# Optimization experiments

Hardware: AMD Instinct MI355X
Metric: run time of the kernel (lower is better)

Reference implementation:

```python
import jax, jax.numpy as jnp
import numpy as np

VIS_DIM = 4096
HIDDEN_D = 4096
EMB_DIM = 512
B = 128
N_NEG = 2048


def setup_inputs() -> dict:
    key = jax.random.key(0)
    k = jax.random.split(key, 7)
    vfs = jax.random.normal(k[0], (B, VIS_DIM), dtype=jnp.float32)
    p_lfs = jax.random.normal(k[1], (B, EMB_DIM), dtype=jnp.float32)
    n_lfs = jax.random.normal(k[2], (N_NEG, EMB_DIM), dtype=jnp.float32)
    # Linear params (PyTorch layout: W [out, in], y = x @ W.T + b)
    s_h = 1.0 / np.sqrt(VIS_DIM)
    s_e = 1.0 / np.sqrt(HIDDEN_D)
    W_h = jax.random.uniform(k[3], (HIDDEN_D, VIS_DIM), jnp.float32, -s_h, s_h)
    b_h = jax.random.uniform(k[4], (HIDDEN_D,), jnp.float32, -s_h, s_h)
    W_e = jax.random.uniform(k[5], (EMB_DIM, HIDDEN_D), jnp.float32, -s_e, s_e)
    b_e = jax.random.uniform(k[6], (EMB_DIM,), jnp.float32, -s_e, s_e)
    return {"vfs": vfs, "p_lfs": p_lfs, "n_lfs": n_lfs,
            "W_h": W_h, "b_h": b_h, "W_e": W_e, "b_e": b_e}


def _partial_order_sim(hypers, hypos):
    # -||relu(hypers - hypos)||_2 reduced over the last axis
    act = jax.nn.relu(hypers - hypos)
    return -jnp.sqrt(jnp.sum(act * act, axis=-1))


def reference(vfs, p_lfs, n_lfs, W_h, b_h, W_e, b_e):
    # Two plain Linears (NO ReLU in between, matching the original forward)
    vf_hidden = vfs @ W_h.T + b_h            # [B, 4096]
    vf_emb = vf_hidden @ W_e.T + b_e          # [B, emb]
    # positive score per sample
    p_scores = _partial_order_sim(p_lfs, vf_emb)                    # [B]
    # negative scores, batched over all samples at once (replaces per-sample loop)
    n_scores = _partial_order_sim(n_lfs[None, :, :], vf_emb[:, None, :])  # [B, N]
    score_stack = jnp.concatenate([p_scores[:, None], n_scores], axis=1)  # [B, N+1]
    return score_stack
```

## Files before the change

### kernel.cpp

```cpp
#include <hip/hip_runtime.h>
#include <hip/hip_bf16.h>

#define B_N  128
#define VIS  4096
#define HID  4096
#define EMB  512
#define NNEG 2048
#define OUTN (NNEG + 1)
#define SPLIT1 8
#define SPLIT2 16

using f32x4  = __attribute__((ext_vector_type(4))) float;
using f32x2  = __attribute__((ext_vector_type(2))) float;
using bf16x8 = __attribute__((ext_vector_type(8))) short;

static __device__ __forceinline__ unsigned pk2bf(float x, float y) {
  union { __hip_bfloat162 h; unsigned u; } c;
  c.h = __float22bfloat162_rn(make_float2(x, y));
  return c.u;
}

#define PIPE_BARRIER() __asm__ volatile("s_waitcnt lgkmcnt(0)\n\ts_barrier" ::: "memory")

__global__ __launch_bounds__(256) void prep_kernel(
    const float* __restrict__ src, unsigned short* __restrict__ dst,
    float* __restrict__ emb) {
  const int idx = blockIdx.x * 256 + threadIdx.x;
  float4 a = ((const float4*)src)[idx * 2];
  float4 b = ((const float4*)src)[idx * 2 + 1];
  uint4 pk;
  pk.x = pk2bf(a.x, a.y); pk.y = pk2bf(a.z, a.w);
  pk.z = pk2bf(b.x, b.y); pk.w = pk2bf(b.z, b.w);
  ((uint4*)dst)[idx] = pk;
  if (idx < (B_N * EMB / 4))
    ((float4*)emb)[idx] = make_float4(0.f, 0.f, 0.f, 0.f);
}

__global__ __launch_bounds__(512, 4) void gemm1_kernel(
    const unsigned short* __restrict__ Abf, const float* __restrict__ Wh,
    const float* __restrict__ bh, float* __restrict__ Hp) {
  const int n0    = blockIdx.x * 64;
  const int kbase = blockIdx.y * 512;

  __shared__ __align__(16) unsigned short Ws[2][64 * 64];

  const int t = threadIdx.x, w = t >> 6, lane = t & 63;
  const int m_lane = lane & 15, kq = lane >> 4;
  f32x4 acc[4] = {};

  const int wr = t >> 3, wg = t & 7;
  const float* Wg = Wh + (size_t)(n0 + wr) * VIS + kbase + wg * 8;
  const int wofs = wr * 64 + ((wg ^ (wr & 7)) * 8);

  const unsigned short* Ag = Abf + (size_t)(w * 16 + m_lane) * VIS + kbase + kq * 8;

  float4 wva[8], wvb[8];
#pragma unroll
  for (int i = 0; i < 8; ++i) {
    wva[i] = *(const float4*)(Wg + i * 64);
    wvb[i] = *(const float4*)(Wg + i * 64 + 4);
  }

  bf16x8 av[3][2];
  av[0][0] = *(const bf16x8*)(Ag);
  av[0][1] = *(const bf16x8*)(Ag + 32);
  av[1][0] = *(const bf16x8*)(Ag + 64);
  av[1][1] = *(const bf16x8*)(Ag + 96);

  {
    uint4 pk;
    pk.x = pk2bf(wva[0].x, wva[0].y); pk.y = pk2bf(wva[0].z, wva[0].w);
    pk.z = pk2bf(wvb[0].x, wvb[0].y); pk.w = pk2bf(wvb[0].z, wvb[0].w);
    *(uint4*)&Ws[0][wofs] = pk;
  }
  PIPE_BARRIER();

#pragma unroll
  for (int k = 0; k < 8; ++k) {
    const int cur = k & 1;
    if (k + 2 < 8) {
      av[(k + 2) % 3][0] = *(const bf16x8*)(Ag + (k + 2) * 64);
      av[(k + 2) % 3][1] = *(const bf16x8*)(Ag + (k + 2) * 64 + 32);
    }
    if (k + 1 < 8) {
      uint4 pk;
      pk.x = pk2bf(wva[k + 1].x, wva[k + 1].y); pk.y = pk2bf(wva[k + 1].z, wva[k + 1].w);
      pk.z = pk2bf(wvb[k + 1].x, wvb[k + 1].y); pk.w = pk2bf(wvb[k + 1].z, wvb[k + 1].w);
      *(uint4*)&Ws[1 - cur][wofs] = pk;
    }
#pragma unroll
    for (int ks = 0; ks < 2; ++ks) {
      const int Gk = ks * 4 + kq;
      const bf16x8 a = av[k % 3][ks];
#pragma unroll
      for (int ni = 0; ni < 4; ++ni) {
        const int c = m_lane + ni * 16;
        bf16x8 b = *(const bf16x8*)&Ws[cur][c * 64 + ((Gk ^ (c & 7)) * 8)];
        acc[ni] = __builtin_amdgcn_mfma_f32_16x16x32_bf16(a, b, acc[ni], 0, 0, 0);
      }
    }
    PIPE_BARRIER();
  }

  float* Pd = Hp + (size_t)blockIdx.y * (B_N * HID);
  const int rq = (lane >> 4) * 4;
#pragma unroll
  for (int ni = 0; ni < 4; ++ni) {
    const int ng = n0 + ni * 16 + m_lane;
    const float bias = (blockIdx.y == 0) ? bh[ng] : 0.0f;
#pragma unroll
    for (int r = 0; r < 4; ++r)
      Pd[(size_t)(w * 16 + rq + r) * HID + ng] = acc[ni][r] + bias;
  }
}

__global__ __launch_bounds__(256) void cvt_kernel(
    const float* __restrict__ Hp, unsigned short* __restrict__ dst) {
  const int idx = blockIdx.x * 256 + threadIdx.x;
  const size_t PS = (size_t)B_N * HID;
  float4 a = ((const float4*)Hp)[idx * 2];
  float4 b = ((const float4*)Hp)[idx * 2 + 1];
#pragma unroll
  for (int p = 1; p < SPLIT1; ++p) {
    float4 ap = ((const float4*)(Hp + p * PS))[idx * 2];
    float4 bp = ((const float4*)(Hp + p * PS))[idx * 2 + 1];
    a.x += ap.x; a.y += ap.y; a.z += ap.z; a.w += ap.w;
    b.x += bp.x; b.y += bp.y; b.z += bp.z; b.w += bp.w;
  }
  uint4 pk;
  pk.x = pk2bf(a.x, a.y); pk.y = pk2bf(a.z, a.w);
  pk.z = pk2bf(b.x, b.y); pk.w = pk2bf(b.z, b.w);
  ((uint4*)dst)[idx] = pk;
}

__global__ __launch_bounds__(512, 4) void gemm2_kernel(
    const unsigned short* __restrict__ Hbf, const float* __restrict__ We,
    const float* __restrict__ be, float* __restrict__ emb) {
  const int n0    = blockIdx.x * 16;
  const int kbase = blockIdx.y * 256;

  __shared__ __align__(16) unsigned short Ws[2][16 * 64];

  const int t = threadIdx.x, w = t >> 6, lane = t & 63;
  const int m_lane = lane & 15, kq = lane >> 4;
  f32x4 acc = {};

  const int wr = t >> 5, e = (t & 31) * 2;
  const float* Wg = We + (size_t)(n0 + wr) * HID + kbase + e;
  const int wofs = wr * 64 + (((e >> 3) ^ (wr & 7)) * 8) + (e & 7);

  const unsigned short* Ag = Hbf + (size_t)(w * 16 + m_lane) * HID + kbase + kq * 8;

  float2 wv[4];
#pragma unroll
  for (int i = 0; i < 4; ++i) wv[i] = *(const float2*)(Wg + i * 64);

  bf16x8 av[3][2];
  av[0][0] = *(const bf16x8*)(Ag);
  av[0][1] = *(const bf16x8*)(Ag + 32);
  av[1][0] = *(const bf16x8*)(Ag + 64);
  av[1][1] = *(const bf16x8*)(Ag + 96);

  *(unsigned*)&Ws[0][wofs] = pk2bf(wv[0].x, wv[0].y);
  PIPE_BARRIER();

#pragma unroll
  for (int k = 0; k < 4; ++k) {
    const int cur = k & 1;
    if (k + 2 < 4) {
      av[(k + 2) % 3][0] = *(const bf16x8*)(Ag + (k + 2) * 64);
      av[(k + 2) % 3][1] = *(const bf16x8*)(Ag + (k + 2) * 64 + 32);
    }
    if (k + 1 < 4) {
      const float2 wc = wv[k + 1];
      *(unsigned*)&Ws[1 - cur][wofs] = pk2bf(wc.x, wc.y);
    }
#pragma unroll
    for (int ks = 0; ks < 2; ++ks) {
      const int Gk = ks * 4 + kq;
      bf16x8 b0 = *(const bf16x8*)&Ws[cur][m_lane * 64 + ((Gk ^ (m_lane & 7)) * 8)];
      acc = __builtin_amdgcn_mfma_f32_16x16x32_bf16(av[k % 3][ks], b0, acc, 0, 0, 0);
    }
    PIPE_BARRIER();
  }

  const int rq = (lane >> 4) * 4;
  const int ng = n0 + m_lane;
  const float bias = (blockIdx.y == 0) ? be[ng] : 0.0f;
#pragma unroll
  for (int r = 0; r < 4; ++r)
    atomicAdd(&emb[(w * 16 + rq + r) * EMB + ng], acc[r] + bias);
}

__global__ __launch_bounds__(256, 2) void score_kernel(
    const float* __restrict__ emb, const float* __restrict__ n_lfs,
    const float* __restrict__ p_lfs, float* __restrict__ out) {
  const int bx = blockIdx.x;
  const int t = threadIdx.x;
  const int s = t & 15, tb = t >> 4;
  const f32x2 z2 = {0.f, 0.f};

  if (bx < 1024) {
    const int nc = bx >> 3, bt = bx & 7;
    const int n0 = nc * 16, b0 = bt * 16;
    __shared__ __align__(16) float nl[16 * 576];
#pragma unroll
    for (int i = 0; i < 8; ++i) {
      const int f = t + i * 256;
      const int r = f >> 7, o4 = f & 127;
      float4 v = *(const float4*)(n_lfs + (size_t)(n0 + r) * EMB + o4 * 4);
      *(float4*)&nl[r * 576 + (o4 >> 3) * 36 + (o4 & 7) * 4] = v;
    }
    const float* eb = emb + (size_t)(b0 + tb) * EMB + s * 32;
    f32x2 ev[16];
#pragma unroll
    for (int i = 0; i < 8; ++i) {
      float4 v = *(const float4*)(eb + i * 4);
      ev[2 * i]     = (f32x2){v.x, v.y};
      ev[2 * i + 1] = (f32x2){v.z, v.w};
    }
    __syncthreads();

    for (int j = 0; j < 16; ++j) {
      const float* nr = &nl[j * 576 + s * 36];
      f32x2 a0 = z2, a1 = z2;
#pragma unroll
      for (int i = 0; i < 8; ++i) {
        float4 nv = *(const float4*)(nr + i * 4);
        f32x2 d0 = (f32x2){nv.x, nv.y} - ev[2 * i];
        f32x2 d1 = (f32x2){nv.z, nv.w} - ev[2 * i + 1];
        d0 = __builtin_elementwise_max(d0, z2);
        d1 = __builtin_elementwise_max(d1, z2);
        a0 = __builtin_elementwise_fma(d0, d0, a0);
        a1 = __builtin_elementwise_fma(d1, d1, a1);
      }
      float ss = (a0.x + a0.y) + (a1.x + a1.y);
      ss += __shfl_xor(ss, 1);
      ss += __shfl_xor(ss, 2);
      ss += __shfl_xor(ss, 4);
      ss += __shfl_xor(ss, 8);
      if (s == 0) out[(size_t)(b0 + tb) * OUTN + 1 + n0 + j] = -sqrtf(ss);
    }
  } else {
    const int b = (bx - 1024) * 16 + tb;
    const float* eb = emb + (size_t)b * EMB + s * 32;
    const float* pb = p_lfs + (size_t)b * EMB + s * 32;
    f32x2 a0 = z2, a1 = z2;
#pragma unroll
    for (int i = 0; i < 8; ++i) {
      float4 pv = *(const float4*)(pb + i * 4);
      float4 ev = *(const float4*)(eb + i * 4);
      f32x2 d0 = (f32x2){pv.x, pv.y} - (f32x2){ev.x, ev.y};
      f32x2 d1 = (f32x2){pv.z, pv.w} - (f32x2){ev.z, ev.w};
      d0 = __builtin_elementwise_max(d0, z2);
      d1 = __builtin_elementwise_max(d1, z2);
      a0 = __builtin_elementwise_fma(d0, d0, a0);
      a1 = __builtin_elementwise_fma(d1, d1, a1);
    }
    float ss = (a0.x + a0.y) + (a1.x + a1.y);
    ss += __shfl_xor(ss, 1);
    ss += __shfl_xor(ss, 2);
    ss += __shfl_xor(ss, 4);
    ss += __shfl_xor(ss, 8);
    if (s == 0) out[(size_t)b * OUTN] = -sqrtf(ss);
  }
}

extern "C" void kernel_launch(void* const* d_in, const int* in_sizes, int n_in,
                              void* d_out, int out_size, void* d_ws, size_t ws_size,
                              hipStream_t stream) {
  const float* vfs   = (const float*)d_in[0];
  const float* p_lfs = (const float*)d_in[1];
  const float* n_lfs = (const float*)d_in[2];
  const float* W_h   = (const float*)d_in[3];
  const float* b_h   = (const float*)d_in[4];
  const float* W_e   = (const float*)d_in[5];
  const float* b_e   = (const float*)d_in[6];
  float* out = (float*)d_out;

  char* ws = (char*)d_ws;
  float*          Hp  = (float*)ws;
  float*          emb = (float*)(ws + (16u << 20));
  unsigned short* Abf = (unsigned short*)(ws + (16u << 20) + (256u << 10));
  unsigned short* Hbf = (unsigned short*)(ws + (17u << 20) + (256u << 10));

  prep_kernel<<<256, 256, 0, stream>>>(vfs, Abf, emb);
  gemm1_kernel<<<dim3(HID / 64, SPLIT1), 512, 0, stream>>>(Abf, W_h, b_h, Hp);
  cvt_kernel<<<256, 256, 0, stream>>>(Hp, Hbf);
  gemm2_kernel<<<dim3(EMB / 16, SPLIT2), 512, 0, stream>>>(Hbf, W_e, b_e, emb);
  score_kernel<<<1032, 256, 0, stream>>>(emb, n_lfs, p_lfs, out);
}
```

Measured before the change: 155.0 us.

## Fuse all five stages into one persistent kernel with grid barriers

Replaces the prep, two GEMM, reduce-convert and score kernels with a single persistent kernel of 512 blocks that separates the stages with atomic-counter grid barriers. A memset resets the barrier counters before each launch. This removes four kernel launch gaps and their tail effects, at the cost of global spin barriers and a deadlock risk if all 512 blocks cannot be resident at once. The score stage is regrouped so each block handles 32 batch rows by 16 negatives, giving 512 blocks.

```diff
diff --git a/kernel.cpp b/kernel.cpp
--- a/kernel.cpp
+++ b/kernel.cpp
@@ -9,6 +9,7 @@
 #define OUTN (NNEG + 1)
 #define SPLIT1 8
 #define SPLIT2 16
+#define NBLK 512u
 
 using f32x4  = __attribute__((ext_vector_type(4))) float;
 using f32x2  = __attribute__((ext_vector_type(2))) float;
@@ -22,191 +23,197 @@
 
 #define PIPE_BARRIER() __asm__ volatile("s_waitcnt lgkmcnt(0)\n\ts_barrier" ::: "memory")
 
-__global__ __launch_bounds__(256) void prep_kernel(
-    const float* __restrict__ src, unsigned short* __restrict__ dst,
-    float* __restrict__ emb) {
-  const int idx = blockIdx.x * 256 + threadIdx.x;
-  float4 a = ((const float4*)src)[idx * 2];
-  float4 b = ((const float4*)src)[idx * 2 + 1];
-  uint4 pk;
-  pk.x = pk2bf(a.x, a.y); pk.y = pk2bf(a.z, a.w);
-  pk.z = pk2bf(b.x, b.y); pk.w = pk2bf(b.z, b.w);
-  ((uint4*)dst)[idx] = pk;
-  if (idx < (B_N * EMB / 4))
-    ((float4*)emb)[idx] = make_float4(0.f, 0.f, 0.f, 0.f);
+static __device__ __forceinline__ void gbar(unsigned* bar, int ph) {
+  __syncthreads();
+  if (threadIdx.x == 0) {
+    __threadfence();
+    __hip_atomic_fetch_add(&bar[ph], 1u, __ATOMIC_RELEASE, __HIP_MEMORY_SCOPE_AGENT);
+    while (__hip_atomic_load(&bar[ph], __ATOMIC_ACQUIRE, __HIP_MEMORY_SCOPE_AGENT) < NBLK)
+      __builtin_amdgcn_s_sleep(2);
+    __threadfence();
+  }
+  __syncthreads();
 }
 
-__global__ __launch_bounds__(512, 4) void gemm1_kernel(
-    const unsigned short* __restrict__ Abf, const float* __restrict__ Wh,
-    const float* __restrict__ bh, float* __restrict__ Hp) {
-  const int n0    = blockIdx.x * 64;
-  const int kbase = blockIdx.y * 512;
-
-  __shared__ __align__(16) unsigned short Ws[2][64 * 64];
-
-  const int t = threadIdx.x, w = t >> 6, lane = t & 63;
-  const int m_lane = lane & 15, kq = lane >> 4;
-  f32x4 acc[4] = {};
-
-  const int wr = t >> 3, wg = t & 7;
-  const float* Wg = Wh + (size_t)(n0 + wr) * VIS + kbase + wg * 8;
-  const int wofs = wr * 64 + ((wg ^ (wr & 7)) * 8);
-
-  const unsigned short* Ag = Abf + (size_t)(w * 16 + m_lane) * VIS + kbase + kq * 8;
-
-  float4 wva[8], wvb[8];
-#pragma unroll
-  for (int i = 0; i < 8; ++i) {
-    wva[i] = *(const float4*)(Wg + i * 64);
-    wvb[i] = *(const float4*)(Wg + i * 64 + 4);
-  }
-
-  bf16x8 av[3][2];
-  av[0][0] = *(const bf16x8*)(Ag);
-  av[0][1] = *(const bf16x8*)(Ag + 32);
-  av[1][0] = *(const bf16x8*)(Ag + 64);
-  av[1][1] = *(const bf16x8*)(Ag + 96);
-
-  {
-    uint4 pk;
-    pk.x = pk2bf(wva[0].x, wva[0].y); pk.y = pk2bf(wva[0].z, wva[0].w);
-    pk.z = pk2bf(wvb[0].x, wvb[0].y); pk.w = pk2bf(wvb[0].z, wvb[0].w);
-    *(uint4*)&Ws[0][wofs] = pk;
-  }
-  PIPE_BARRIER();
-
-#pragma unroll
-  for (int k = 0; k < 8; ++k) {
-    const int cur = k & 1;
-    if (k + 2 < 8) {
-      av[(k + 2) % 3][0] = *(const bf16x8*)(Ag + (k + 2) * 64);
-      av[(k + 2) % 3][1] = *(const bf16x8*)(Ag + (k + 2) * 64 + 32);
-    }
-    if (k + 1 < 8) {
+__global__ __launch_bounds__(512, 4) void mega_kernel(
+    const float* __restrict__ vfs, const float* __restrict__ p_lfs,
+    const float* __restrict__ n_lfs, const float* __restrict__ Wh,
+    const float* __restrict__ bh, const float* __restrict__ We,
+    const float* __restrict__ be, float* __restrict__ out,
+    float* __restrict__ Hp, float* __restrict__ emb,
+    unsigned short* __restrict__ Abf, unsigned short* __restrict__ Hbf,
+    unsigned* __restrict__ bar) {
+
+  __shared__ __align__(16) char smem[16 * 576 * 4];
+
+  const int bid = blockIdx.x, t = threadIdx.x;
+  const int gid = bid * 512 + t;
+
+  {
+    float2 a = ((const float2*)vfs)[gid];
+    ((unsigned*)Abf)[gid] = pk2bf(a.x, a.y);
+    if (gid < (B_N * EMB / 4))
+      ((float4*)emb)[gid] = make_float4(0.f, 0.f, 0.f, 0.f);
+  }
+  gbar(bar, 0);
+
+  {
+    const int bx = bid & 63, by = bid >> 6;
+    const int n0    = bx * 64;
+    const int kbase = by * 512;
+    unsigned short* Wsb = (unsigned short*)smem;
+
+    const int w = t >> 6, lane = t & 63;
+    const int m_lane = lane & 15, kq = lane >> 4;
+    f32x4 acc[4] = {};
+
+    const int wr = t >> 3, wg = t & 7;
+    const float* Wg = Wh + (size_t)(n0 + wr) * VIS + kbase + wg * 8;
+    const int wofs = wr * 64 + ((wg ^ (wr & 7)) * 8);
+
+    const unsigned short* Ag = Abf + (size_t)(w * 16 + m_lane) * VIS + kbase + kq * 8;
+
+    float4 wva[8], wvb[8];
+#pragma unroll
+    for (int i = 0; i < 8; ++i) {
+      wva[i] = *(const float4*)(Wg + i * 64);
+      wvb[i] = *(const float4*)(Wg + i * 64 + 4);
+    }
+
+    bf16x8 av[3][2];
+    av[0][0] = *(const bf16x8*)(Ag);
+    av[0][1] = *(const bf16x8*)(Ag + 32);
+    av[1][0] = *(const bf16x8*)(Ag + 64);
+    av[1][1] = *(const bf16x8*)(Ag + 96);
+
+    {
       uint4 pk;
-      pk.x = pk2bf(wva[k + 1].x, wva[k + 1].y); pk.y = pk2bf(wva[k + 1].z, wva[k + 1].w);
-      pk.z = pk2bf(wvb[k + 1].x, wvb[k + 1].y); pk.w = pk2bf(wvb[k + 1].z, wvb[k + 1].w);
-      *(uint4*)&Ws[1 - cur][wofs] = pk;
-    }
-#pragma unroll
-    for (int ks = 0; ks < 2; ++ks) {
-      const int Gk = ks * 4 + kq;
-      const bf16x8 a = av[k % 3][ks];
-#pragma unroll
-      for (int ni = 0; ni < 4; ++ni) {
-        const int c = m_lane + ni * 16;
-        bf16x8 b = *(const bf16x8*)&Ws[cur][c * 64 + ((Gk ^ (c & 7)) * 8)];
-        acc[ni] = __builtin_amdgcn_mfma_f32_16x16x32_bf16(a, b, acc[ni], 0, 0, 0);
-      }
+      pk.x = pk2bf(wva[0].x, wva[0].y); pk.y = pk2bf(wva[0].z, wva[0].w);
+      pk.z = pk2bf(wvb[0].x, wvb[0].y); pk.w = pk2bf(wvb[0].z, wvb[0].w);
+      *(uint4*)&Wsb[wofs] = pk;
     }
     PIPE_BARRIER();
-  }
-
-  float* Pd = Hp + (size_t)blockIdx.y * (B_N * HID);
-  const int rq = (lane >> 4) * 4;
-#pragma unroll
-  for (int ni = 0; ni < 4; ++ni) {
-    const int ng = n0 + ni * 16 + m_lane;
-    const float bias = (blockIdx.y == 0) ? bh[ng] : 0.0f;
+
+#pragma unroll
+    for (int k = 0; k < 8; ++k) {
+      const int cur = k & 1;
+      if (k + 2 < 8) {
+        av[(k + 2) % 3][0] = *(const bf16x8*)(Ag + (k + 2) * 64);
+        av[(k + 2) % 3][1] = *(const bf16x8*)(Ag + (k + 2) * 64 + 32);
+      }
+      if (k + 1 < 8) {
+        uint4 pk;
+        pk.x = pk2bf(wva[k + 1].x, wva[k + 1].y); pk.y = pk2bf(wva[k + 1].z, wva[k + 1].w);
+        pk.z = pk2bf(wvb[k + 1].x, wvb[k + 1].y); pk.w = pk2bf(wvb[k + 1].z, wvb[k + 1].w);
+        *(uint4*)&Wsb[(1 - cur) * 4096 + wofs] = pk;
+      }
+#pragma unroll
+      for (int ks = 0; ks < 2; ++ks) {
+        const int Gk = ks * 4 + kq;
+        const bf16x8 a = av[k % 3][ks];
+#pragma unroll
+        for (int ni = 0; ni < 4; ++ni) {
+          const int c = m_lane + ni * 16;
+          bf16x8 b = *(const bf16x8*)&Wsb[cur * 4096 + c * 64 + ((Gk ^ (c & 7)) * 8)];
+          acc[ni] = __builtin_amdgcn_mfma_f32_16x16x32_bf16(a, b, acc[ni], 0, 0, 0);
+        }
+      }
+      PIPE_BARRIER();
+    }
+
+    float* Pd = Hp + (size_t)by * (B_N * HID);
+    const int rq = (lane >> 4) * 4;
+#pragma unroll
+    for (int ni = 0; ni < 4; ++ni) {
+      const int ng = n0 + ni * 16 + m_lane;
+      const float bias = (by == 0) ? bh[ng] : 0.0f;
+#pragma unroll
+      for (int r = 0; r < 4; ++r)
+        Pd[(size_t)(w * 16 + rq + r) * HID + ng] = acc[ni][r] + bias;
+    }
+  }
+  gbar(bar, 1);
+
+  {
+    const size_t PS2 = (size_t)B_N * HID / 2;
+    const float2* hp2 = (const float2*)Hp;
+    float2 a = hp2[gid];
+#pragma unroll
+    for (int p = 1; p < SPLIT1; ++p) {
+      float2 v = hp2[gid + p * PS2];
+      a.x += v.x; a.y += v.y;
+    }
+    ((unsigned*)Hbf)[gid] = pk2bf(a.x, a.y);
+  }
+  gbar(bar, 2);
+
+  {
+    const int bx = bid & 31, by = bid >> 5;
+    const int n0    = bx * 16;
+    const int kbase = by * 256;
+    unsigned short* Wsb = (unsigned short*)smem;
+
+    const int w = t >> 6, lane = t & 63;
+    const int m_lane = lane & 15, kq = lane >> 4;
+    f32x4 acc = {};
+
+    const int wr = t >> 5, e = (t & 31) * 2;
+    const float* Wg = We + (size_t)(n0 + wr) * HID + kbase + e;
+    const int wofs = wr * 64 + (((e >> 3) ^ (wr & 7)) * 8) + (e & 7);
+
+    const unsigned short* Ag = Hbf + (size_t)(w * 16 + m_lane) * HID + kbase + kq * 8;
+
+    float2 wv[4];
+#pragma unroll
+    for (int i = 0; i < 4; ++i) wv[i] = *(const float2*)(Wg + i * 64);
+
+    bf16x8 av[3][2];
+    av[0][0] = *(const bf16x8*)(Ag);
+    av[0][1] = *(const bf16x8*)(Ag + 32);
+    av[1][0] = *(const bf16x8*)(Ag + 64);
+    av[1][1] = *(const bf16x8*)(Ag + 96);
+
+    *(unsigned*)&Wsb[wofs] = pk2bf(wv[0].x, wv[0].y);
+    PIPE_BARRIER();
+
+#pragma unroll
+    for (int k = 0; k < 4; ++k) {
+      const int cur = k & 1;
+      if (k + 2 < 4) {
+        av[(k + 2) % 3][0] = *(const bf16x8*)(Ag + (k + 2) * 64);
+        av[(k + 2) % 3][1] = *(const bf16x8*)(Ag + (k + 2) * 64 + 32);
+      }
+      if (k + 1 < 4) {
+        const float2 wc = wv[k + 1];
+        *(unsigned*)&Wsb[(1 - cur) * 1024 + wofs] = pk2bf(wc.x, wc.y);
+      }
+#pragma unroll
+      for (int ks = 0; ks < 2; ++ks) {
+        const int Gk = ks * 4 + kq;
+        bf16x8 b0 = *(const bf16x8*)&Wsb[cur * 1024 + m_lane * 64 + ((Gk ^ (m_lane & 7)) * 8)];
+        acc = __builtin_amdgcn_mfma_f32_16x16x32_bf16(av[k % 3][ks], b0, acc, 0, 0, 0);
+      }
+      PIPE_BARRIER();
+    }
+
+    const int rq = (lane >> 4) * 4;
+    const int ng = n0 + m_lane;
+    const float bias = (by == 0) ? be[ng] : 0.0f;
 #pragma unroll
     for (int r = 0; r < 4; ++r)
-      Pd[(size_t)(w * 16 + rq + r) * HID + ng] = acc[ni][r] + bias;
-  }
-}
-
-__global__ __launch_bounds__(256) void cvt_kernel(
-    const float* __restrict__ Hp, unsigned short* __restrict__ dst) {
-  const int idx = blockIdx.x * 256 + threadIdx.x;
-  const size_t PS = (size_t)B_N * HID;
-  float4 a = ((const float4*)Hp)[idx * 2];
-  float4 b = ((const float4*)Hp)[idx * 2 + 1];
-#pragma unroll
-  for (int p = 1; p < SPLIT1; ++p) {
-    float4 ap = ((const float4*)(Hp + p * PS))[idx * 2];
-    float4 bp = ((const float4*)(Hp + p * PS))[idx * 2 + 1];
-    a.x += ap.x; a.y += ap.y; a.z += ap.z; a.w += ap.w;
-    b.x += bp.x; b.y += bp.y; b.z += bp.z; b.w += bp.w;
-  }
-  uint4 pk;
-  pk.x = pk2bf(a.x, a.y); pk.y = pk2bf(a.z, a.w);
-  pk.z = pk2bf(b.x, b.y); pk.w = pk2bf(b.z, b.w);
-  ((uint4*)dst)[idx] = pk;
-}
-
-__global__ __launch_bounds__(512, 4) void gemm2_kernel(
-    const unsigned short* __restrict__ Hbf, const float* __restrict__ We,
-    const float* __restrict__ be, float* __restrict__ emb) {
-  const int n0    = blockIdx.x * 16;
-  const int kbase = blockIdx.y * 256;
-
-  __shared__ __align__(16) unsigned short Ws[2][16 * 64];
-
-  const int t = threadIdx.x, w = t >> 6, lane = t & 63;
-  const int m_lane = lane & 15, kq = lane >> 4;
-  f32x4 acc = {};
-
-  const int wr = t >> 5, e = (t & 31) * 2;
-  const float* Wg = We + (size_t)(n0 + wr) * HID + kbase + e;
-  const int wofs = wr * 64 + (((e >> 3) ^ (wr & 7)) * 8) + (e & 7);
-
-  const unsigned short* Ag = Hbf + (size_t)(w * 16 + m_lane) * HID + kbase + kq * 8;
-
-  float2 wv[4];
-#pragma unroll
-  for (int i = 0; i < 4; ++i) wv[i] = *(const float2*)(Wg + i * 64);
-
-  bf16x8 av[3][2];
-  av[0][0] = *(const bf16x8*)(Ag);
-  av[0][1] = *(const bf16x8*)(Ag + 32);
-  av[1][0] = *(const bf16x8*)(Ag + 64);
-  av[1][1] = *(const bf16x8*)(Ag + 96);
-
-  *(unsigned*)&Ws[0][wofs] = pk2bf(wv[0].x, wv[0].y);
-  PIPE_BARRIER();
-
-#pragma unroll
-  for (int k = 0; k < 4; ++k) {
-    const int cur = k & 1;
-    if (k + 2 < 4) {
-      av[(k + 2) % 3][0] = *(const bf16x8*)(Ag + (k + 2) * 64);
-      av[(k + 2) % 3][1] = *(const bf16x8*)(Ag + (k + 2) * 64 + 32);
-    }
-    if (k + 1 < 4) {
-      const float2 wc = wv[k + 1];
-      *(unsigned*)&Ws[1 - cur][wofs] = pk2bf(wc.x, wc.y);
-    }
-#pragma unroll
-    for (int ks = 0; ks < 2; ++ks) {
-      const int Gk = ks * 4 + kq;
-      bf16x8 b0 = *(const bf16x8*)&Ws[cur][m_lane * 64 + ((Gk ^ (m_lane & 7)) * 8)];
-      acc = __builtin_amdgcn_mfma_f32_16x16x32_bf16(av[k % 3][ks], b0, acc, 0, 0, 0);
-    }
-    PIPE_BARRIER();
-  }
-
-  const int rq = (lane >> 4) * 4;
-  const int ng = n0 + m_lane;
-  const float bias = (blockIdx.y == 0) ? be[ng] : 0.0f;
-#pragma unroll
-  for (int r = 0; r < 4; ++r)
-    atomicAdd(&emb[(w * 16 + rq + r) * EMB + ng], acc[r] + bias);
-}
-
-__global__ __launch_bounds__(256, 2) void score_kernel(
-    const float* __restrict__ emb, const float* __restrict__ n_lfs,
-    const float* __restrict__ p_lfs, float* __restrict__ out) {
-  const int bx = blockIdx.x;
-  const int t = threadIdx.x;
-  const int s = t & 15, tb = t >> 4;
-  const f32x2 z2 = {0.f, 0.f};
-
-  if (bx < 1024) {
-    const int nc = bx >> 3, bt = bx & 7;
-    const int n0 = nc * 16, b0 = bt * 16;
-    __shared__ __align__(16) float nl[16 * 576];
-#pragma unroll
-    for (int i = 0; i < 8; ++i) {
-      const int f = t + i * 256;
+      atomicAdd(&emb[(w * 16 + rq + r) * EMB + ng], acc[r] + bias);
+  }
+  gbar(bar, 3);
+
+  {
+    float* nl = (float*)smem;
+    const int s = t & 15, tb = t >> 4;
+    const int n0 = (bid >> 2) * 16, b0 = (bid & 3) * 32;
+    const f32x2 z2 = {0.f, 0.f};
+
+#pragma unroll
+    for (int i = 0; i < 4; ++i) {
+      const int f = t + i * 512;
       const int r = f >> 7, o4 = f & 127;
       float4 v = *(const float4*)(n_lfs + (size_t)(n0 + r) * EMB + o4 * 4);
       *(float4*)&nl[r * 576 + (o4 >> 3) * 36 + (o4 & 7) * 4] = v;
@@ -241,28 +248,30 @@
       ss += __shfl_xor(ss, 8);
       if (s == 0) out[(size_t)(b0 + tb) * OUTN + 1 + n0 + j] = -sqrtf(ss);
     }
-  } else {
-    const int b = (bx - 1024) * 16 + tb;
-    const float* eb = emb + (size_t)b * EMB + s * 32;
-    const float* pb = p_lfs + (size_t)b * EMB + s * 32;
-    f32x2 a0 = z2, a1 = z2;
-#pragma unroll
-    for (int i = 0; i < 8; ++i) {
-      float4 pv = *(const float4*)(pb + i * 4);
-      float4 ev = *(const float4*)(eb + i * 4);
-      f32x2 d0 = (f32x2){pv.x, pv.y} - (f32x2){ev.x, ev.y};
-      f32x2 d1 = (f32x2){pv.z, pv.w} - (f32x2){ev.z, ev.w};
-      d0 = __builtin_elementwise_max(d0, z2);
-      d1 = __builtin_elementwise_max(d1, z2);
-      a0 = __builtin_elementwise_fma(d0, d0, a0);
-      a1 = __builtin_elementwise_fma(d1, d1, a1);
-    }
-    float ss = (a0.x + a0.y) + (a1.x + a1.y);
-    ss += __shfl_xor(ss, 1);
-    ss += __shfl_xor(ss, 2);
-    ss += __shfl_xor(ss, 4);
-    ss += __shfl_xor(ss, 8);
-    if (s == 0) out[(size_t)b * OUTN] = -sqrtf(ss);
+
+    if (bid < 8 && tb < 16) {
+      const int b = bid * 16 + tb;
+      const float* pb = p_lfs + (size_t)b * EMB + s * 32;
+      const float* ebp = emb + (size_t)b * EMB + s * 32;
+      f32x2 a0 = z2, a1 = z2;
+#pragma unroll
+      for (int i = 0; i < 8; ++i) {
+        float4 pv = *(const float4*)(pb + i * 4);
+        float4 evv = *(const float4*)(ebp + i * 4);
+        f32x2 d0 = (f32x2){pv.x, pv.y} - (f32x2){evv.x, evv.y};
+        f32x2 d1 = (f32x2){pv.z, pv.w} - (f32x2){evv.z, evv.w};
+        d0 = __builtin_elementwise_max(d0, z2);
+        d1 = __builtin_elementwise_max(d1, z2);
+        a0 = __builtin_elementwise_fma(d0, d0, a0);
+        a1 = __builtin_elementwise_fma(d1, d1, a1);
+      }
+      float ss = (a0.x + a0.y) + (a1.x + a1.y);
+      ss += __shfl_xor(ss, 1);
+      ss += __shfl_xor(ss, 2);
+      ss += __shfl_xor(ss, 4);
+      ss += __shfl_xor(ss, 8);
+      if (s == 0) out[(size_t)b * OUTN] = -sqrtf(ss);
+    }
   }
 }
 
@@ -283,10 +292,9 @@
   float*          emb = (float*)(ws + (16u << 20));
   unsigned short* Abf = (unsigned short*)(ws + (16u << 20) + (256u << 10));
   unsigned short* Hbf = (unsigned short*)(ws + (17u << 20) + (256u << 10));
-
-  prep_kernel<<<256, 256, 0, stream>>>(vfs, Abf, emb);
-  gemm1_kernel<<<dim3(HID / 64, SPLIT1), 512, 0, stream>>>(Abf, W_h, b_h, Hp);
-  cvt_kernel<<<256, 256, 0, stream>>>(Hp, Hbf);
-  gemm2_kernel<<<dim3(EMB / 16, SPLIT2), 512, 0, stream>>>(Hbf, W_e, b_e, emb);
-  score_kernel<<<1032, 256, 0, stream>>>(emb, n_lfs, p_lfs, out);
+  unsigned*       bar = (unsigned*)(ws + (18u << 20) + (256u << 10));
+
+  hipMemsetAsync(bar, 0, 4 * sizeof(unsigned), stream);
+  mega_kernel<<<NBLK, 512, 0, stream>>>(vfs, p_lfs, n_lfs, W_h, b_h, W_e, b_e,
+                                        out, Hp, emb, Abf, Hbf, bar);
 }
```

Measured after the change: 451.4 us. +191.1%, slower.
